# Kernel tuning notes

Hardware: AMD Instinct MI355X
Metric: run time of the kernel (lower is better)

The kernel has to match this reference:

```python
import jax, jax.numpy as jnp
import numpy as np

B, IN_DIM, HID = 8192, 1024, 1024

def setup_inputs() -> dict:
    key = jax.random.key(0)
    ks = jax.random.split(key, 11)
    s_in = 1.0 / np.sqrt(IN_DIM + HID)  # torch Linear default init scale
    inp = {
        "Z": jax.random.normal(ks[0], (B, IN_DIM), dtype=jnp.float32),
        "h_prev": jax.random.normal(ks[1], (B, HID), dtype=jnp.float32),
        "c_prev": jax.random.normal(ks[2], (B, HID), dtype=jnp.float32),
        "W_i": jax.random.uniform(ks[3], (IN_DIM + HID, HID), jnp.float32, -s_in, s_in),
        "b_i": jax.random.uniform(ks[4], (HID,), jnp.float32, -s_in, s_in),
        "W_f": jax.random.uniform(ks[5], (IN_DIM + HID, HID), jnp.float32, -s_in, s_in),
        "b_f": jax.random.uniform(ks[6], (HID,), jnp.float32, -s_in, s_in),
        "W_o": jax.random.uniform(ks[7], (IN_DIM + HID, HID), jnp.float32, -s_in, s_in),
        "b_o": jax.random.uniform(ks[8], (HID,), jnp.float32, -s_in, s_in),
        "W_g": jax.random.uniform(ks[9], (IN_DIM + HID, HID), jnp.float32, -s_in, s_in),
        "b_g": jax.random.uniform(ks[10], (HID,), jnp.float32, -s_in, s_in),
    }
    return inp

def reference(Z, h_prev, c_prev, W_i, b_i, W_f, b_f, W_o, b_o, W_g, b_g):
    combined = jnp.concatenate([Z, h_prev], axis=1)  # [B, IN+HID]
    i = jax.nn.sigmoid(combined @ W_i + b_i)
    f = jax.nn.sigmoid(combined @ W_f + b_f)
    o = jax.nn.sigmoid(combined @ W_o + b_o)
    g = jnp.tanh(combined @ W_g + b_g)
    c = f * c_prev + i * g
    h = o * jnp.tanh(c)
    return (h, c)
```

## Files before the change

### kernel.cpp

```cpp
#include <hip/hip_runtime.h>


#define BDIM 8192
#define KDIM 2048
#define NDIM 1024
#define NCAT 4096
#define NT   32

typedef __bf16 bf16x8 __attribute__((ext_vector_type(8)));
typedef float  f32x4  __attribute__((ext_vector_type(4)));

__device__ __forceinline__ void async_cp16(const void* g, void* l) {
    __builtin_amdgcn_global_load_lds((__attribute__((address_space(1))) void*)g,
                                     (__attribute__((address_space(3))) void*)l,
                                     16, 0, 0);
}

__device__ __forceinline__ float sigm(float x) { return 1.f / (1.f + __expf(-x)); }
__device__ __forceinline__ float tanh_fast(float x) { return 1.f - 2.f / (1.f + __expf(2.f * x)); }

#define BARM asm volatile("s_barrier" ::: "memory")

__global__ __launch_bounds__(256)
void prep_kernel(const float* __restrict__ Z, const float* __restrict__ H,
                 const float* __restrict__ Wi, const float* __restrict__ Wf,
                 const float* __restrict__ Wo, const float* __restrict__ Wg,
                 __bf16* __restrict__ A, __bf16* __restrict__ Wt) {
    __shared__ float t[64][65];
    const int bid = blockIdx.x;
    const int tid = threadIdx.x;

    if (bid < 8192) {
        const bool isZ = (bid < 4096);
        const int idx  = (isZ ? bid : bid - 4096) * 256 + tid;
        const int row  = idx >> 7;
        const int q8   = idx & 127;
        const float* src = isZ ? Z : H;
        const float4* p = (const float4*)src + ((size_t)row << 8) + q8 * 2;
        float4 v0 = p[0], v1 = p[1];
        bf16x8 o = { (__bf16)v0.x, (__bf16)v0.y, (__bf16)v0.z, (__bf16)v0.w,
                     (__bf16)v1.x, (__bf16)v1.y, (__bf16)v1.z, (__bf16)v1.w };
        const int col8 = isZ ? q8 : (q8 + 128);
        ((bf16x8*)A)[(size_t)row * 256 + col8] = o;
    } else {
        const int id  = bid - 8192;
        const int g   = id >> 9;
        const int rem = id & 511;
        const int k0  = (rem & 31) * 64;
        const int n0  = (rem >> 5) * 64;
        const float* W = (g == 0) ? Wi : (g == 1) ? Wf : (g == 2) ? Wo : Wg;

        const int c4 = tid & 15, r0 = tid >> 4;
        #pragma unroll
        for (int it = 0; it < 4; ++it) {
            const int r = r0 + it * 16;
            float4 v = ((const float4*)W)[(size_t)(k0 + r) * 256 + (n0 >> 2) + c4];
            t[r][c4 * 4 + 0] = v.x;
            t[r][c4 * 4 + 1] = v.y;
            t[r][c4 * 4 + 2] = v.z;
            t[r][c4 * 4 + 3] = v.w;
        }
        __syncthreads();

        const int kc = tid & 7, nn0 = tid >> 3;
        #pragma unroll
        for (int j = 0; j < 2; ++j) {
            const int n    = nn0 + j * 32;
            const int ncat = n0 + n;
            const size_t outRow = (size_t)(ncat >> 5) * 128 + g * 32 + (ncat & 31);
            bf16x8 o;
            #pragma unroll
            for (int kk = 0; kk < 8; ++kk) o[kk] = (__bf16)t[kc * 8 + kk][n];
            *(bf16x8*)(Wt + outRow * KDIM + k0 + kc * 8) = o;
        }
    }
}

__global__ __launch_bounds__(512, 2)
void lstm_gemm_kernel(const __bf16* __restrict__ A, const __bf16* __restrict__ Wt,
                      const float* __restrict__ b_i, const float* __restrict__ b_f,
                      const float* __restrict__ b_o, const float* __restrict__ b_g,
                      const float* __restrict__ c_prev, float* __restrict__ out) {
    extern __shared__ char smem[];

    const int tid  = threadIdx.x;
    const int wave = tid >> 6;
    const int lane = tid & 63;
    const int wm   = wave >> 2;
    const int wn   = wave & 3;
    const int l15  = lane & 15;
    const int quad = lane >> 4;

    const int bid = blockIdx.x;
    const int bxc = (bid & 7) * 2 + (bid >> 8);
    const int by  = (bid >> 3) & 31;
    const int m0   = by * 256;
    const int cat0 = bxc * 256;
    const int n0   = bxc * 64;

    const int srow = tid >> 2;
    const int sgch = (tid & 3) ^ ((tid >> 3) & 3);
    const __bf16* Ags = A  + (size_t)(m0   + srow) * KDIM + sgch * 8;
    const __bf16* Bgs = Wt + (size_t)(cat0 + srow) * KDIM + sgch * 8;
    char* ldsw = smem + wave * 1024;

#define STG(o, h, kt, b) do { \
    const __bf16* gp_ = ((o) ? Bgs : Ags) + (size_t)(h) * 128 * KDIM + (kt) * 64; \
    char* lp_ = ldsw + (b) * 65536 + (o) * 32768 + (h) * 16384; \
    async_cp16(gp_,      lp_); \
    async_cp16(gp_ + 32, lp_ + 8192); \
} while (0)

    const int swz   = (quad ^ ((l15 >> 1) & 3)) * 16;
    const int abase = wm * 16384 + l15 * 64 + swz;
    const int bbase = 32768 + (wn >> 1) * 16384 + ((wn & 1) * 64 + l15) * 64 + swz;

    f32x4 acc[8][4];
    #pragma unroll
    for (int i = 0; i < 8; ++i)
        #pragma unroll
        for (int j = 0; j < 4; ++j) acc[i][j] = (f32x4){0.f, 0.f, 0.f, 0.f};

    bf16x8 af[4][2];
    bf16x8 bf[4][2];

    auto LDA = [&](int mh, int bufb) {
        const char* p = smem + bufb + abase + mh * 4096;
        #pragma unroll
        for (int m = 0; m < 4; ++m) {
            af[m][0] = *(const bf16x8*)(p + m * 1024);
            af[m][1] = *(const bf16x8*)(p + m * 1024 + 8192);
        }
    };
    auto LDB = [&](int nh, int bufb) {
        const char* p = smem + bufb + bbase + nh * 2048;
        #pragma unroll
        for (int n = 0; n < 2; ++n) {
            bf[nh * 2 + n][0] = *(const bf16x8*)(p + n * 1024);
            bf[nh * 2 + n][1] = *(const bf16x8*)(p + n * 1024 + 8192);
        }
    };
    auto MMA = [&](int mh, int nh) {
        #pragma unroll
        for (int m = 0; m < 4; ++m)
            #pragma unroll
            for (int n = 0; n < 2; ++n) {
                acc[mh * 4 + m][nh * 2 + n] = __builtin_amdgcn_mfma_f32_16x16x32_bf16(
                    af[m][0], bf[nh * 2 + n][0], acc[mh * 4 + m][nh * 2 + n], 0, 0, 0);
                acc[mh * 4 + m][nh * 2 + n] = __builtin_amdgcn_mfma_f32_16x16x32_bf16(
                    af[m][1], bf[nh * 2 + n][1], acc[mh * 4 + m][nh * 2 + n], 0, 0, 0);
            }
    };

    STG(0, 0, 0, 0); STG(1, 0, 0, 0); STG(0, 1, 0, 0); STG(1, 1, 0, 0);
    STG(0, 0, 1, 1); STG(1, 0, 1, 1);
    asm volatile("s_waitcnt vmcnt(4)" ::: "memory");
    BARM;

    #pragma unroll 2
    for (int t = 0; t < NT; ++t) {
        const int b    = t & 1;
        const int bufb = b * 65536;
        LDA(0, bufb); LDB(0, bufb);
        if (t + 1 < NT) STG(0, 1, t + 1, b ^ 1);
        BARM; asm volatile("s_waitcnt lgkmcnt(0)" ::: "memory");
        __builtin_amdgcn_s_setprio(1); MMA(0, 0); __builtin_amdgcn_s_setprio(0);
        BARM;
        LDB(1, bufb);
        if (t + 1 < NT) STG(1, 1, t + 1, b ^ 1);
        BARM; asm volatile("s_waitcnt lgkmcnt(0)" ::: "memory");
        __builtin_amdgcn_s_setprio(1); MMA(0, 1); __builtin_amdgcn_s_setprio(0);
        BARM;
        LDA(1, bufb);
        BARM; asm volatile("s_waitcnt lgkmcnt(0)" ::: "memory");
        __builtin_amdgcn_s_setprio(1); MMA(1, 0); __builtin_amdgcn_s_setprio(0);
        BARM;
        if (t + 2 < NT) { STG(0, 0, t + 2, b); STG(1, 0, t + 2, b); }
        if (t < NT - 2) { asm volatile("s_waitcnt vmcnt(4)" ::: "memory"); }
        else            { asm volatile("s_waitcnt vmcnt(0)" ::: "memory"); }
        BARM;
        __builtin_amdgcn_s_setprio(1); MMA(1, 1); __builtin_amdgcn_s_setprio(0);
        BARM;
    }

    float* Ep = (float*)smem;
    const int nn = tid & 63;
    const float bvi = b_i[n0 + nn], bvf = b_f[n0 + nn];
    const float bvo = b_o[n0 + nn], bvg = b_g[n0 + nn];
    int colW[4];
    #pragma unroll
    for (int nt = 0; nt < 4; ++nt)
        colW[nt] = ((wn & 1) * 2 + (nt >> 1)) * 64 + (wn >> 1) * 32 + (nt & 1) * 16 + l15;

    #pragma unroll
    for (int ch = 0; ch < 4; ++ch) {
        __syncthreads();
        if (wm == (ch >> 1)) {
            #pragma unroll
            for (int mi = 0; mi < 4; ++mi) {
                const int mt = (ch & 1) * 4 + mi;
                #pragma unroll
                for (int nt = 0; nt < 4; ++nt)
                    #pragma unroll
                    for (int r = 0; r < 4; ++r)
                        Ep[(mi * 16 + quad * 4 + r) * 258 + colW[nt]] = acc[mt][nt][r];
            }
        }
        __syncthreads();
        #pragma unroll
        for (int e = 0; e < 8; ++e) {
            const int row = e * 8 + wave;
            const float gi = sigm(Ep[row * 258 + nn] + bvi);
            const float gf = sigm(Ep[row * 258 + 64 + nn] + bvf);
            const float go = sigm(Ep[row * 258 + 128 + nn] + bvo);
            const float gg = tanh_fast(Ep[row * 258 + 192 + nn] + bvg);
            const size_t pos = (size_t)(m0 + ch * 64 + row) * NDIM + n0 + nn;
            const float cp = c_prev[pos];
            const float cv = gf * cp + gi * gg;
            out[pos] = go * tanh_fast(cv);
            out[(size_t)BDIM * NDIM + pos] = cv;
        }
    }
#undef STG
}

extern "C" void kernel_launch(void* const* d_in, const int* in_sizes, int n_in,
                              void* d_out, int out_size, void* d_ws, size_t ws_size,
                              hipStream_t stream) {
    const float* Z  = (const float*)d_in[0];
    const float* H  = (const float*)d_in[1];
    const float* Cp = (const float*)d_in[2];
    const float* Wi = (const float*)d_in[3];
    const float* bi = (const float*)d_in[4];
    const float* Wf = (const float*)d_in[5];
    const float* bf = (const float*)d_in[6];
    const float* Wo = (const float*)d_in[7];
    const float* bo = (const float*)d_in[8];
    const float* Wg = (const float*)d_in[9];
    const float* bg = (const float*)d_in[10];

    __bf16* Acomb = (__bf16*)d_ws;
    __bf16* Wt    = (__bf16*)((char*)d_ws + (size_t)33554432);

    static bool cfg = false;
    if (!cfg) {
        hipFuncSetAttribute(reinterpret_cast<const void*>(lstm_gemm_kernel),
                            hipFuncAttributeMaxDynamicSharedMemorySize, 131072);
        cfg = true;
    }

    prep_kernel<<<10240, 256, 0, stream>>>(Z, H, Wi, Wf, Wo, Wg, Acomb, Wt);
    lstm_gemm_kernel<<<512, 512, 131072, stream>>>(
        Acomb, Wt, bi, bf, bo, bg, Cp, (float*)d_out);
}
```

Measured before the change: 319.7 us.

## Switch GEMM mainloop to triple-buffered K=32 stages with one barrier per step

After: 329.1 us. 2.9% more time.

```diff
diff --git a/kernel.cpp b/kernel.cpp
--- a/kernel.cpp
+++ b/kernel.cpp
@@ -5,7 +5,7 @@
 #define KDIM 2048
 #define NDIM 1024
 #define NCAT 4096
-#define NT   32
+#define NK   64
 
 typedef __bf16 bf16x8 __attribute__((ext_vector_type(8)));
 typedef float  f32x4  __attribute__((ext_vector_type(4)));
@@ -104,16 +104,16 @@
     const __bf16* Bgs = Wt + (size_t)(cat0 + srow) * KDIM + sgch * 8;
     char* ldsw = smem + wave * 1024;
 
-#define STG(o, h, kt, b) do { \
-    const __bf16* gp_ = ((o) ? Bgs : Ags) + (size_t)(h) * 128 * KDIM + (kt) * 64; \
-    char* lp_ = ldsw + (b) * 65536 + (o) * 32768 + (h) * 16384; \
-    async_cp16(gp_,      lp_); \
-    async_cp16(gp_ + 32, lp_ + 8192); \
+#define STG(o, kt, s) do { \
+    const __bf16* gp_ = ((o) ? Bgs : Ags) + (size_t)(kt) * 32; \
+    char* lp_ = ldsw + (s) * 32768 + (o) * 16384; \
+    async_cp16(gp_, lp_); \
+    async_cp16(gp_ + (size_t)128 * KDIM, lp_ + 8192); \
 } while (0)
 
     const int swz   = (quad ^ ((l15 >> 1) & 3)) * 16;
-    const int abase = wm * 16384 + l15 * 64 + swz;
-    const int bbase = 32768 + (wn >> 1) * 16384 + ((wn & 1) * 64 + l15) * 64 + swz;
+    const int abase = (wm * 128 + l15) * 64 + swz;
+    const int bbase = 16384 + ((wn >> 1) * 128 + (wn & 1) * 64 + l15) * 64 + swz;
 
     f32x4 acc[8][4];
     #pragma unroll
@@ -121,66 +121,35 @@
         #pragma unroll
         for (int j = 0; j < 4; ++j) acc[i][j] = (f32x4){0.f, 0.f, 0.f, 0.f};
 
-    bf16x8 af[4][2];
-    bf16x8 bf[4][2];
-
-    auto LDA = [&](int mh, int bufb) {
-        const char* p = smem + bufb + abase + mh * 4096;
-        #pragma unroll
-        for (int m = 0; m < 4; ++m) {
-            af[m][0] = *(const bf16x8*)(p + m * 1024);
-            af[m][1] = *(const bf16x8*)(p + m * 1024 + 8192);
-        }
-    };
-    auto LDB = [&](int nh, int bufb) {
-        const char* p = smem + bufb + bbase + nh * 2048;
-        #pragma unroll
-        for (int n = 0; n < 2; ++n) {
-            bf[nh * 2 + n][0] = *(const bf16x8*)(p + n * 1024);
-            bf[nh * 2 + n][1] = *(const bf16x8*)(p + n * 1024 + 8192);
-        }
-    };
-    auto MMA = [&](int mh, int nh) {
-        #pragma unroll
-        for (int m = 0; m < 4; ++m)
-            #pragma unroll
-            for (int n = 0; n < 2; ++n) {
-                acc[mh * 4 + m][nh * 2 + n] = __builtin_amdgcn_mfma_f32_16x16x32_bf16(
-                    af[m][0], bf[nh * 2 + n][0], acc[mh * 4 + m][nh * 2 + n], 0, 0, 0);
-                acc[mh * 4 + m][nh * 2 + n] = __builtin_amdgcn_mfma_f32_16x16x32_bf16(
-                    af[m][1], bf[nh * 2 + n][1], acc[mh * 4 + m][nh * 2 + n], 0, 0, 0);
-            }
-    };
-
-    STG(0, 0, 0, 0); STG(1, 0, 0, 0); STG(0, 1, 0, 0); STG(1, 1, 0, 0);
-    STG(0, 0, 1, 1); STG(1, 0, 1, 1);
+    STG(0, 0, 0); STG(1, 0, 0);
+    STG(0, 1, 1); STG(1, 1, 1);
     asm volatile("s_waitcnt vmcnt(4)" ::: "memory");
     BARM;
 
-    #pragma unroll 2
-    for (int t = 0; t < NT; ++t) {
-        const int b    = t & 1;
-        const int bufb = b * 65536;
-        LDA(0, bufb); LDB(0, bufb);
-        if (t + 1 < NT) STG(0, 1, t + 1, b ^ 1);
-        BARM; asm volatile("s_waitcnt lgkmcnt(0)" ::: "memory");
-        __builtin_amdgcn_s_setprio(1); MMA(0, 0); __builtin_amdgcn_s_setprio(0);
-        BARM;
-        LDB(1, bufb);
-        if (t + 1 < NT) STG(1, 1, t + 1, b ^ 1);
-        BARM; asm volatile("s_waitcnt lgkmcnt(0)" ::: "memory");
-        __builtin_amdgcn_s_setprio(1); MMA(0, 1); __builtin_amdgcn_s_setprio(0);
-        BARM;
-        LDA(1, bufb);
-        BARM; asm volatile("s_waitcnt lgkmcnt(0)" ::: "memory");
-        __builtin_amdgcn_s_setprio(1); MMA(1, 0); __builtin_amdgcn_s_setprio(0);
-        BARM;
-        if (t + 2 < NT) { STG(0, 0, t + 2, b); STG(1, 0, t + 2, b); }
-        if (t < NT - 2) { asm volatile("s_waitcnt vmcnt(4)" ::: "memory"); }
+    int cur = 0;
+    for (int t = 0; t < NK; ++t) {
+        int stg = cur - 1; if (stg < 0) stg = 2;
+        if (t + 2 < NK) { STG(0, t + 2, stg); STG(1, t + 2, stg); }
+
+        const char* bp = smem + cur * 32768;
+        bf16x8 af[8], bfr[4];
+        #pragma unroll
+        for (int mi = 0; mi < 8; ++mi) af[mi]  = *(const bf16x8*)(bp + abase + mi * 1024);
+        #pragma unroll
+        for (int nt = 0; nt < 4; ++nt) bfr[nt] = *(const bf16x8*)(bp + bbase + nt * 1024);
+
+        __builtin_amdgcn_s_setprio(1);
+        #pragma unroll
+        for (int mi = 0; mi < 8; ++mi)
+            #pragma unroll
+            for (int nt = 0; nt < 4; ++nt)
+                acc[mi][nt] = __builtin_amdgcn_mfma_f32_16x16x32_bf16(af[mi], bfr[nt], acc[mi][nt], 0, 0, 0);
+        __builtin_amdgcn_s_setprio(0);
+
+        if (t < NK - 2) { asm volatile("s_waitcnt vmcnt(4)" ::: "memory"); }
         else            { asm volatile("s_waitcnt vmcnt(0)" ::: "memory"); }
         BARM;
-        __builtin_amdgcn_s_setprio(1); MMA(1, 1); __builtin_amdgcn_s_setprio(0);
-        BARM;
+        ++cur; if (cur == 3) cur = 0;
     }
 
     float* Ep = (float*)smem;
@@ -245,11 +214,11 @@
     static bool cfg = false;
     if (!cfg) {
         hipFuncSetAttribute(reinterpret_cast<const void*>(lstm_gemm_kernel),
-                            hipFuncAttributeMaxDynamicSharedMemorySize, 131072);
+                            hipFuncAttributeMaxDynamicSharedMemorySize, 98304);
         cfg = true;
     }
 
     prep_kernel<<<10240, 256, 0, stream>>>(Z, H, Wi, Wf, Wo, Wg, Acomb, Wt);
-    lstm_gemm_kernel<<<512, 512, 131072, stream>>>(
+    lstm_gemm_kernel<<<512, 512, 98304, stream>>>(
         Acomb, Wt, bi, bf, bo, bg, Cp, (float*)d_out);
 }
```

## Fuse prep into persistent GEMM kernel with grid barrier and two M-tiles per block

Applied to the files above, without the earlier changes.

Result: slower. 466.7 us (+46.0%).

```diff
diff --git a/kernel.cpp b/kernel.cpp
--- a/kernel.cpp
+++ b/kernel.cpp
@@ -76,14 +76,77 @@
     }
 }
 
+template<bool PREP>
 __global__ __launch_bounds__(512, 2)
-void lstm_gemm_kernel(const __bf16* __restrict__ A, const __bf16* __restrict__ Wt,
-                      const float* __restrict__ b_i, const float* __restrict__ b_f,
-                      const float* __restrict__ b_o, const float* __restrict__ b_g,
-                      const float* __restrict__ c_prev, float* __restrict__ out) {
+void fused_lstm(const float* __restrict__ Z, const float* __restrict__ H,
+                const float* __restrict__ c_prev,
+                const float* __restrict__ Wi, const float* __restrict__ Wf,
+                const float* __restrict__ Wo, const float* __restrict__ Wg,
+                const float* __restrict__ b_i, const float* __restrict__ b_f,
+                const float* __restrict__ b_o, const float* __restrict__ b_g,
+                __bf16* __restrict__ A, __bf16* __restrict__ Wt,
+                unsigned* __restrict__ bar, float* __restrict__ out) {
     extern __shared__ char smem[];
 
-    const int tid  = threadIdx.x;
+    const int tid = threadIdx.x;
+    const int bid = blockIdx.x;
+
+    if constexpr (PREP) {
+        const int gtid = bid * 512 + tid;
+        #pragma unroll
+        for (int t = 0; t < 16; ++t) {
+            const int u    = gtid + t * 131072;
+            const int row  = u >> 8;
+            const int col8 = u & 255;
+            const float* src = (col8 < 128) ? Z : H;
+            const int q8 = col8 & 127;
+            const float4* p = (const float4*)src + ((size_t)row << 8) + q8 * 2;
+            float4 v0 = p[0], v1 = p[1];
+            bf16x8 o = { (__bf16)v0.x, (__bf16)v0.y, (__bf16)v0.z, (__bf16)v0.w,
+                         (__bf16)v1.x, (__bf16)v1.y, (__bf16)v1.z, (__bf16)v1.w };
+            ((bf16x8*)A)[(size_t)row * 256 + col8] = o;
+        }
+
+        float* tt = (float*)smem;
+        const int c4 = tid & 15, r0 = tid >> 4;
+        const int kc = tid & 7,  nn2 = tid >> 3;
+        #pragma unroll 1
+        for (int it = 0; it < 8; ++it) {
+            const int id  = bid * 8 + it;
+            const int g   = id >> 9;
+            const int rem = id & 511;
+            const int k0  = (rem & 31) * 64;
+            const int n0t = (rem >> 5) * 64;
+            const float* W = (g == 0) ? Wi : (g == 1) ? Wf : (g == 2) ? Wo : Wg;
+            __syncthreads();
+            #pragma unroll
+            for (int j = 0; j < 2; ++j) {
+                const int r = r0 + j * 32;
+                float4 v = ((const float4*)W)[(size_t)(k0 + r) * 256 + (n0t >> 2) + c4];
+                tt[r * 65 + c4 * 4 + 0] = v.x;
+                tt[r * 65 + c4 * 4 + 1] = v.y;
+                tt[r * 65 + c4 * 4 + 2] = v.z;
+                tt[r * 65 + c4 * 4 + 3] = v.w;
+            }
+            __syncthreads();
+            const int ncat = n0t + nn2;
+            const size_t outRow = (size_t)(ncat >> 5) * 128 + g * 32 + (ncat & 31);
+            bf16x8 o;
+            #pragma unroll
+            for (int kk = 0; kk < 8; ++kk) o[kk] = (__bf16)tt[(kc * 8 + kk) * 65 + nn2];
+            *(bf16x8*)(Wt + outRow * KDIM + k0 + kc * 8) = o;
+        }
+
+        __syncthreads();
+        __threadfence();
+        if (tid == 0) {
+            atomicAdd(bar, 1u);
+            while (atomicAdd(bar, 0u) < 256u) __builtin_amdgcn_s_sleep(2);
+        }
+        __syncthreads();
+        __threadfence();
+    }
+
     const int wave = tid >> 6;
     const int lane = tid & 63;
     const int wm   = wave >> 2;
@@ -91,21 +154,24 @@
     const int l15  = lane & 15;
     const int quad = lane >> 4;
 
-    const int bid = blockIdx.x;
-    const int bxc = (bid & 7) * 2 + (bid >> 8);
-    const int by  = (bid >> 3) & 31;
-    const int m0   = by * 256;
+    const int xcd = bid & 7;
+    const int j   = bid >> 3;
+    const int bxc = xcd * 2 + (j & 1);
+    const int by0 = j >> 1;
+    const int m0a  = by0 * 256;
+    const int m0b  = m0a + 4096;
     const int cat0 = bxc * 256;
-    const int n0   = bxc * 64;
+    const int n0c  = bxc * 64;
 
     const int srow = tid >> 2;
     const int sgch = (tid & 3) ^ ((tid >> 3) & 3);
-    const __bf16* Ags = A  + (size_t)(m0   + srow) * KDIM + sgch * 8;
-    const __bf16* Bgs = Wt + (size_t)(cat0 + srow) * KDIM + sgch * 8;
+    const __bf16* AgsA = A  + (size_t)(m0a  + srow) * KDIM + sgch * 8;
+    const __bf16* AgsB = AgsA + (size_t)4096 * KDIM;
+    const __bf16* Bgs  = Wt + (size_t)(cat0 + srow) * KDIM + sgch * 8;
     char* ldsw = smem + wave * 1024;
 
-#define STG(o, h, kt, b) do { \
-    const __bf16* gp_ = ((o) ? Bgs : Ags) + (size_t)(h) * 128 * KDIM + (kt) * 64; \
+#define STG(AP, o, h, kt, b) do { \
+    const __bf16* gp_ = ((o) ? Bgs : (AP)) + (size_t)(h) * 128 * KDIM + (kt) * 64; \
     char* lp_ = ldsw + (b) * 65536 + (o) * 32768 + (h) * 16384; \
     async_cp16(gp_,      lp_); \
     async_cp16(gp_ + 32, lp_ + 8192); \
@@ -113,31 +179,26 @@
 
     const int swz   = (quad ^ ((l15 >> 1) & 3)) * 16;
     const int abase = wm * 16384 + l15 * 64 + swz;
-    const int bbase = 32768 + (wn >> 1) * 16384 + ((wn & 1) * 64 + l15) * 64 + swz;
+    const int bbase = 32768 + (wn >> 1) * 16384 + (wn & 1) * 4096 + l15 * 64 + swz;
 
     f32x4 acc[8][4];
-    #pragma unroll
-    for (int i = 0; i < 8; ++i)
-        #pragma unroll
-        for (int j = 0; j < 4; ++j) acc[i][j] = (f32x4){0.f, 0.f, 0.f, 0.f};
-
-    bf16x8 af[4][2];
-    bf16x8 bf[4][2];
+    bf16x8 afr[4][2];
+    bf16x8 bfr[4][2];
 
     auto LDA = [&](int mh, int bufb) {
         const char* p = smem + bufb + abase + mh * 4096;
         #pragma unroll
         for (int m = 0; m < 4; ++m) {
-            af[m][0] = *(const bf16x8*)(p + m * 1024);
-            af[m][1] = *(const bf16x8*)(p + m * 1024 + 8192);
+            afr[m][0] = *(const bf16x8*)(p + m * 1024);
+            afr[m][1] = *(const bf16x8*)(p + m * 1024 + 8192);
         }
     };
     auto LDB = [&](int nh, int bufb) {
         const char* p = smem + bufb + bbase + nh * 2048;
         #pragma unroll
         for (int n = 0; n < 2; ++n) {
-            bf[nh * 2 + n][0] = *(const bf16x8*)(p + n * 1024);
-            bf[nh * 2 + n][1] = *(const bf16x8*)(p + n * 1024 + 8192);
+            bfr[nh * 2 + n][0] = *(const bf16x8*)(p + n * 1024);
+            bfr[nh * 2 + n][1] = *(const bf16x8*)(p + n * 1024 + 8192);
         }
     };
     auto MMA = [&](int mh, int nh) {
@@ -146,82 +207,114 @@
             #pragma unroll
             for (int n = 0; n < 2; ++n) {
                 acc[mh * 4 + m][nh * 2 + n] = __builtin_amdgcn_mfma_f32_16x16x32_bf16(
-                    af[m][0], bf[nh * 2 + n][0], acc[mh * 4 + m][nh * 2 + n], 0, 0, 0);
+                    afr[m][0], bfr[nh * 2 + n][0], acc[mh * 4 + m][nh * 2 + n], 0, 0, 0);
                 acc[mh * 4 + m][nh * 2 + n] = __builtin_amdgcn_mfma_f32_16x16x32_bf16(
-                    af[m][1], bf[nh * 2 + n][1], acc[mh * 4 + m][nh * 2 + n], 0, 0, 0);
+                    afr[m][1], bfr[nh * 2 + n][1], acc[mh * 4 + m][nh * 2 + n], 0, 0, 0);
             }
     };
 
-    STG(0, 0, 0, 0); STG(1, 0, 0, 0); STG(0, 1, 0, 0); STG(1, 1, 0, 0);
-    STG(0, 0, 1, 1); STG(1, 0, 1, 1);
-    asm volatile("s_waitcnt vmcnt(4)" ::: "memory");
-    BARM;
-
-    #pragma unroll 2
-    for (int t = 0; t < NT; ++t) {
-        const int b    = t & 1;
-        const int bufb = b * 65536;
-        LDA(0, bufb); LDB(0, bufb);
-        if (t + 1 < NT) STG(0, 1, t + 1, b ^ 1);
-        BARM; asm volatile("s_waitcnt lgkmcnt(0)" ::: "memory");
-        __builtin_amdgcn_s_setprio(1); MMA(0, 0); __builtin_amdgcn_s_setprio(0);
-        BARM;
-        LDB(1, bufb);
-        if (t + 1 < NT) STG(1, 1, t + 1, b ^ 1);
-        BARM; asm volatile("s_waitcnt lgkmcnt(0)" ::: "memory");
-        __builtin_amdgcn_s_setprio(1); MMA(0, 1); __builtin_amdgcn_s_setprio(0);
-        BARM;
-        LDA(1, bufb);
-        BARM; asm volatile("s_waitcnt lgkmcnt(0)" ::: "memory");
-        __builtin_amdgcn_s_setprio(1); MMA(1, 0); __builtin_amdgcn_s_setprio(0);
-        BARM;
-        if (t + 2 < NT) { STG(0, 0, t + 2, b); STG(1, 0, t + 2, b); }
-        if (t < NT - 2) { asm volatile("s_waitcnt vmcnt(4)" ::: "memory"); }
-        else            { asm volatile("s_waitcnt vmcnt(0)" ::: "memory"); }
-        BARM;
-        __builtin_amdgcn_s_setprio(1); MMA(1, 1); __builtin_amdgcn_s_setprio(0);
-        BARM;
-    }
-
-    float* Ep = (float*)smem;
+#define ZERO_ACC do { \
+    _Pragma("unroll") \
+    for (int i = 0; i < 8; ++i) \
+        _Pragma("unroll") \
+        for (int jj = 0; jj < 4; ++jj) acc[i][jj] = (f32x4){0.f, 0.f, 0.f, 0.f}; \
+} while (0)
+
+#define KLOOP(AP) do { \
+    _Pragma("unroll 2") \
+    for (int t = 0; t < NT; ++t) { \
+        const int b    = t & 1; \
+        const int bufb = b * 65536; \
+        LDA(0, bufb); LDB(0, bufb); \
+        if (t + 1 < NT) STG(AP, 0, 1, t + 1, b ^ 1); \
+        BARM; asm volatile("s_waitcnt lgkmcnt(0)" ::: "memory"); \
+        __builtin_amdgcn_s_setprio(1); MMA(0, 0); __builtin_amdgcn_s_setprio(0); \
+        BARM; \
+        LDB(1, bufb); \
+        if (t + 1 < NT) STG(AP, 1, 1, t + 1, b ^ 1); \
+        BARM; asm volatile("s_waitcnt lgkmcnt(0)" ::: "memory"); \
+        __builtin_amdgcn_s_setprio(1); MMA(0, 1); __builtin_amdgcn_s_setprio(0); \
+        BARM; \
+        LDA(1, bufb); \
+        BARM; asm volatile("s_waitcnt lgkmcnt(0)" ::: "memory"); \
+        __builtin_amdgcn_s_setprio(1); MMA(1, 0); __builtin_amdgcn_s_setprio(0); \
+        BARM; \
+        if (t + 2 < NT) { STG(AP, 0, 0, t + 2, b); STG(AP, 1, 0, t + 2, b); } \
+        if (t < NT - 2) { asm volatile("s_waitcnt vmcnt(4)" ::: "memory"); } \
+        else            { asm volatile("s_waitcnt vmcnt(0)" ::: "memory"); } \
+        BARM; \
+        __builtin_amdgcn_s_setprio(1); MMA(1, 1); __builtin_amdgcn_s_setprio(0); \
+        BARM; \
+    } \
+} while (0)
+
     const int nn = tid & 63;
-    const float bvi = b_i[n0 + nn], bvf = b_f[n0 + nn];
-    const float bvo = b_o[n0 + nn], bvg = b_g[n0 + nn];
+    const float bvi = b_i[n0c + nn], bvf = b_f[n0c + nn];
+    const float bvo = b_o[n0c + nn], bvg = b_g[n0c + nn];
     int colW[4];
     #pragma unroll
     for (int nt = 0; nt < 4; ++nt)
         colW[nt] = ((wn & 1) * 2 + (nt >> 1)) * 64 + (wn >> 1) * 32 + (nt & 1) * 16 + l15;
 
-    #pragma unroll
-    for (int ch = 0; ch < 4; ++ch) {
-        __syncthreads();
-        if (wm == (ch >> 1)) {
-            #pragma unroll
-            for (int mi = 0; mi < 4; ++mi) {
-                const int mt = (ch & 1) * 4 + mi;
-                #pragma unroll
-                for (int nt = 0; nt < 4; ++nt)
-                    #pragma unroll
-                    for (int r = 0; r < 4; ++r)
-                        Ep[(mi * 16 + quad * 4 + r) * 258 + colW[nt]] = acc[mt][nt][r];
-            }
-        }
-        __syncthreads();
-        #pragma unroll
-        for (int e = 0; e < 8; ++e) {
-            const int row = e * 8 + wave;
-            const float gi = sigm(Ep[row * 258 + nn] + bvi);
-            const float gf = sigm(Ep[row * 258 + 64 + nn] + bvf);
-            const float go = sigm(Ep[row * 258 + 128 + nn] + bvo);
-            const float gg = tanh_fast(Ep[row * 258 + 192 + nn] + bvg);
-            const size_t pos = (size_t)(m0 + ch * 64 + row) * NDIM + n0 + nn;
-            const float cp = c_prev[pos];
-            const float cv = gf * cp + gi * gg;
-            out[pos] = go * tanh_fast(cv);
-            out[(size_t)BDIM * NDIM + pos] = cv;
-        }
-    }
+#define EPI(m0v) do { \
+    float* Ep = (float*)(smem + 94208); \
+    _Pragma("unroll 1") \
+    for (int ch = 0; ch < 8; ++ch) { \
+        __syncthreads(); \
+        if (wm == (ch >> 2)) { \
+            _Pragma("unroll") \
+            for (int mi2 = 0; mi2 < 2; ++mi2) { \
+                const int mt = (ch & 3) * 2 + mi2; \
+                _Pragma("unroll") \
+                for (int nt = 0; nt < 4; ++nt) \
+                    _Pragma("unroll") \
+                    for (int r = 0; r < 4; ++r) \
+                        Ep[(mi2 * 16 + quad * 4 + r) * 258 + colW[nt]] = acc[mt][nt][r]; \
+            } \
+        } \
+        __syncthreads(); \
+        _Pragma("unroll") \
+        for (int e = 0; e < 4; ++e) { \
+            const int idx = tid + e * 512; \
+            const int row = idx >> 6; \
+            const float gi = sigm(Ep[row * 258 + nn] + bvi); \
+            const float gf = sigm(Ep[row * 258 + 64 + nn] + bvf); \
+            const float go = sigm(Ep[row * 258 + 128 + nn] + bvo); \
+            const float gg = tanh_fast(Ep[row * 258 + 192 + nn] + bvg); \
+            const size_t pos = (size_t)((m0v) + ch * 32 + row) * NDIM + n0c + nn; \
+            const float cp = c_prev[pos]; \
+            const float cv = gf * cp + gi * gg; \
+            out[pos] = go * tanh_fast(cv); \
+            out[(size_t)BDIM * NDIM + pos] = cv; \
+        } \
+    } \
+} while (0)
+
+    ZERO_ACC;
+    STG(AgsA, 0, 0, 0, 0); STG(AgsA, 1, 0, 0, 0);
+    STG(AgsA, 0, 1, 0, 0); STG(AgsA, 1, 1, 0, 0);
+    STG(AgsA, 0, 0, 1, 1); STG(AgsA, 1, 0, 1, 1);
+    asm volatile("s_waitcnt vmcnt(4)" ::: "memory");
+    BARM;
+    KLOOP(AgsA);
+
+    STG(AgsB, 0, 0, 0, 0); STG(AgsB, 1, 0, 0, 0);
+    STG(AgsB, 0, 1, 0, 0); STG(AgsB, 1, 1, 0, 0);
+
+    EPI(m0a);
+    __syncthreads();
+
+    ZERO_ACC;
+    STG(AgsB, 0, 0, 1, 1); STG(AgsB, 1, 0, 1, 1);
+    asm volatile("s_waitcnt vmcnt(4)" ::: "memory");
+    BARM;
+    KLOOP(AgsB);
+    EPI(m0b);
+
 #undef STG
+#undef KLOOP
+#undef EPI
+#undef ZERO_ACC
 }
 
 extern "C" void kernel_launch(void* const* d_in, const int* in_sizes, int n_in,
@@ -238,18 +331,30 @@
     const float* bo = (const float*)d_in[8];
     const float* Wg = (const float*)d_in[9];
     const float* bg = (const float*)d_in[10];
-
-    __bf16* Acomb = (__bf16*)d_ws;
-    __bf16* Wt    = (__bf16*)((char*)d_ws + (size_t)33554432);
+    float* outp = (float*)d_out;
 
     static bool cfg = false;
     if (!cfg) {
-        hipFuncSetAttribute(reinterpret_cast<const void*>(lstm_gemm_kernel),
+        hipFuncSetAttribute(reinterpret_cast<const void*>(fused_lstm<true>),
+                            hipFuncAttributeMaxDynamicSharedMemorySize, 131072);
+        hipFuncSetAttribute(reinterpret_cast<const void*>(fused_lstm<false>),
                             hipFuncAttributeMaxDynamicSharedMemorySize, 131072);
         cfg = true;
     }
 
-    prep_kernel<<<10240, 256, 0, stream>>>(Z, H, Wi, Wf, Wo, Wg, Acomb, Wt);
-    lstm_gemm_kernel<<<512, 512, 131072, stream>>>(
-        Acomb, Wt, bi, bf, bo, bg, Cp, (float*)d_out);
+    const size_t need = (size_t)4096 + 33554432 + 16777216;
+    if (ws_size >= need) {
+        unsigned* bar = (unsigned*)d_ws;
+        __bf16* Acomb = (__bf16*)((char*)d_ws + 4096);
+        __bf16* Wtp   = (__bf16*)((char*)d_ws + 4096 + (size_t)33554432);
+        hipMemsetAsync(d_ws, 0, 64, stream);
+        fused_lstm<true><<<256, 512, 131072, stream>>>(
+            Z, H, Cp, Wi, Wf, Wo, Wg, bi, bf, bo, bg, Acomb, Wtp, bar, outp);
+    } else {
+        __bf16* Acomb = (__bf16*)d_ws;
+        __bf16* Wtp   = (__bf16*)((char*)d_ws + (size_t)33554432);
+        prep_kernel<<<10240, 256, 0, stream>>>(Z, H, Wi, Wf, Wo, Wg, Acomb, Wtp);
+        fused_lstm<false><<<256, 512, 131072, stream>>>(
+            Z, H, Cp, Wi, Wf, Wo, Wg, bi, bf, bo, bg, Acomb, Wtp, nullptr, outp);
+    }
 }
```

## Switch GEMM inner loop from 16x16x32 to 32x32x16 bf16 MFMA tiles

Applied to the files above, without the earlier changes.

Result: slower. 387.5 us (+21.2%).

```diff
diff --git a/kernel.cpp b/kernel.cpp
--- a/kernel.cpp
+++ b/kernel.cpp
@@ -9,6 +9,7 @@
 
 typedef __bf16 bf16x8 __attribute__((ext_vector_type(8)));
 typedef float  f32x4  __attribute__((ext_vector_type(4)));
+typedef float  f32x16 __attribute__((ext_vector_type(16)));
 
 __device__ __forceinline__ void async_cp16(const void* g, void* l) {
     __builtin_amdgcn_global_load_lds((__attribute__((address_space(1))) void*)g,
@@ -88,15 +89,15 @@
     const int lane = tid & 63;
     const int wm   = wave >> 2;
     const int wn   = wave & 3;
-    const int l15  = lane & 15;
-    const int quad = lane >> 4;
+    const int l31  = lane & 31;
+    const int lh   = lane >> 5;
 
     const int bid = blockIdx.x;
     const int bxc = (bid & 7) * 2 + (bid >> 8);
     const int by  = (bid >> 3) & 31;
     const int m0   = by * 256;
     const int cat0 = bxc * 256;
-    const int n0   = bxc * 64;
+    const int n0c  = bxc * 64;
 
     const int srow = tid >> 2;
     const int sgch = (tid & 3) ^ ((tid >> 3) & 3);
@@ -111,45 +112,46 @@
     async_cp16(gp_ + 32, lp_ + 8192); \
 } while (0)
 
-    const int swz   = (quad ^ ((l15 >> 1) & 3)) * 16;
-    const int abase = wm * 16384 + l15 * 64 + swz;
-    const int bbase = 32768 + (wn >> 1) * 16384 + ((wn & 1) * 64 + l15) * 64 + swz;
-
-    f32x4 acc[8][4];
+    const int rowb = l31 * 64;
+    int achk[4];
     #pragma unroll
-    for (int i = 0; i < 8; ++i)
-        #pragma unroll
-        for (int j = 0; j < 4; ++j) acc[i][j] = (f32x4){0.f, 0.f, 0.f, 0.f};
-
-    bf16x8 af[4][2];
-    bf16x8 bf[4][2];
+    for (int ki = 0; ki < 4; ++ki)
+        achk[ki] = (ki >> 1) * 8192 + (((2 * (ki & 1) + lh) ^ ((lane >> 1) & 3)) * 16);
+    const int abase = wm * 16384 + rowb;
+    const int bbase = 32768 + (wn >> 1) * 16384 + (wn & 1) * 4096 + rowb;
+
+    f32x16 acc[4][2];
+    #pragma unroll
+    for (int i = 0; i < 4; ++i)
+        #pragma unroll
+        for (int j = 0; j < 2; ++j)
+            #pragma unroll
+            for (int r = 0; r < 16; ++r) acc[i][j][r] = 0.f;
+
+    bf16x8 af[2][4];
+    bf16x8 bfr[2][4];
 
     auto LDA = [&](int mh, int bufb) {
         const char* p = smem + bufb + abase + mh * 4096;
         #pragma unroll
-        for (int m = 0; m < 4; ++m) {
-            af[m][0] = *(const bf16x8*)(p + m * 1024);
-            af[m][1] = *(const bf16x8*)(p + m * 1024 + 8192);
-        }
+        for (int mi = 0; mi < 2; ++mi)
+            #pragma unroll
+            for (int ki = 0; ki < 4; ++ki)
+                af[mi][ki] = *(const bf16x8*)(p + mi * 2048 + achk[ki]);
     };
     auto LDB = [&](int nh, int bufb) {
         const char* p = smem + bufb + bbase + nh * 2048;
         #pragma unroll
-        for (int n = 0; n < 2; ++n) {
-            bf[nh * 2 + n][0] = *(const bf16x8*)(p + n * 1024);
-            bf[nh * 2 + n][1] = *(const bf16x8*)(p + n * 1024 + 8192);
-        }
+        for (int ki = 0; ki < 4; ++ki)
+            bfr[nh][ki] = *(const bf16x8*)(p + achk[ki]);
     };
     auto MMA = [&](int mh, int nh) {
         #pragma unroll
-        for (int m = 0; m < 4; ++m)
-            #pragma unroll
-            for (int n = 0; n < 2; ++n) {
-                acc[mh * 4 + m][nh * 2 + n] = __builtin_amdgcn_mfma_f32_16x16x32_bf16(
-                    af[m][0], bf[nh * 2 + n][0], acc[mh * 4 + m][nh * 2 + n], 0, 0, 0);
-                acc[mh * 4 + m][nh * 2 + n] = __builtin_amdgcn_mfma_f32_16x16x32_bf16(
-                    af[m][1], bf[nh * 2 + n][1], acc[mh * 4 + m][nh * 2 + n], 0, 0, 0);
-            }
+        for (int ki = 0; ki < 4; ++ki)
+            #pragma unroll
+            for (int mi = 0; mi < 2; ++mi)
+                acc[mh * 2 + mi][nh] = __builtin_amdgcn_mfma_f32_32x32x16_bf16(
+                    af[mi][ki], bfr[nh][ki], acc[mh * 2 + mi][nh], 0, 0, 0);
     };
 
     STG(0, 0, 0, 0); STG(1, 0, 0, 0); STG(0, 1, 0, 0); STG(1, 1, 0, 0);
@@ -185,36 +187,37 @@
 
     float* Ep = (float*)smem;
     const int nn = tid & 63;
-    const float bvi = b_i[n0 + nn], bvf = b_f[n0 + nn];
-    const float bvo = b_o[n0 + nn], bvg = b_g[n0 + nn];
-    int colW[4];
+    const float bvi = b_i[n0c + nn], bvf = b_f[n0c + nn];
+    const float bvo = b_o[n0c + nn], bvg = b_g[n0c + nn];
+    int colW[2];
     #pragma unroll
-    for (int nt = 0; nt < 4; ++nt)
-        colW[nt] = ((wn & 1) * 2 + (nt >> 1)) * 64 + (wn >> 1) * 32 + (nt & 1) * 16 + l15;
-
-    #pragma unroll
-    for (int ch = 0; ch < 4; ++ch) {
+    for (int nt = 0; nt < 2; ++nt) {
+        const int q = 2 * wn + nt;
+        colW[nt] = ((q & 3) << 6) + ((q >> 2) << 5) + l31;
+    }
+
+    #pragma unroll 1
+    for (int ch = 0; ch < 8; ++ch) {
         __syncthreads();
-        if (wm == (ch >> 1)) {
-            #pragma unroll
-            for (int mi = 0; mi < 4; ++mi) {
-                const int mt = (ch & 1) * 4 + mi;
+        if (wm == (ch >> 2)) {
+            const int mt = ch & 3;
+            #pragma unroll
+            for (int nt = 0; nt < 2; ++nt)
                 #pragma unroll
-                for (int nt = 0; nt < 4; ++nt)
-                    #pragma unroll
-                    for (int r = 0; r < 4; ++r)
-                        Ep[(mi * 16 + quad * 4 + r) * 258 + colW[nt]] = acc[mt][nt][r];
-            }
+                for (int r = 0; r < 16; ++r)
+                    Ep[((r & 3) + ((r >> 2) << 3) + (lh << 2)) * 258 + colW[nt]] =
+                        acc[mt][nt][r];
         }
         __syncthreads();
         #pragma unroll
-        for (int e = 0; e < 8; ++e) {
-            const int row = e * 8 + wave;
+        for (int e = 0; e < 4; ++e) {
+            const int idx = tid + e * 512;
+            const int row = idx >> 6;
             const float gi = sigm(Ep[row * 258 + nn] + bvi);
             const float gf = sigm(Ep[row * 258 + 64 + nn] + bvf);
             const float go = sigm(Ep[row * 258 + 128 + nn] + bvo);
             const float gg = tanh_fast(Ep[row * 258 + 192 + nn] + bvg);
-            const size_t pos = (size_t)(m0 + ch * 64 + row) * NDIM + n0 + nn;
+            const size_t pos = (size_t)(m0 + ch * 32 + row) * NDIM + n0c + nn;
             const float cp = c_prev[pos];
             const float cv = gf * cp + gi * gg;
             out[pos] = go * tanh_fast(cv);
@@ -240,7 +243,7 @@
     const float* bg = (const float*)d_in[10];
 
     __bf16* Acomb = (__bf16*)d_ws;
-    __bf16* Wt    = (__bf16*)((char*)d_ws + (size_t)33554432);
+    __bf16* Wtp   = (__bf16*)((char*)d_ws + (size_t)33554432);
 
     static bool cfg = false;
     if (!cfg) {
@@ -249,7 +252,7 @@
         cfg = true;
     }
 
-    prep_kernel<<<10240, 256, 0, stream>>>(Z, H, Wi, Wf, Wo, Wg, Acomb, Wt);
+    prep_kernel<<<10240, 256, 0, stream>>>(Z, H, Wi, Wf, Wo, Wg, Acomb, Wtp);
     lstm_gemm_kernel<<<512, 512, 131072, stream>>>(
-        Acomb, Wt, bi, bf, bo, bg, Cp, (float*)d_out);
-}
+        Acomb, Wtp, bi, bf, bo, bg, Cp, (float*)d_out);
+}
```
